# Optimization experiments

Hardware: AMD Instinct MI355X
Metric: run time of the kernel (lower is better)

## Reference

```python
import jax, jax.numpy as jnp
import numpy as np

B, S, D, H = 4, 2048, 1024, 16
Dh = D // H
MAX_WAVELENGTH = 10000.0


def apply_rope(x, positions, head_dim):
    # x: [B, S, H, Dh], positions: [B, S]
    fraction = 2.0 * jnp.arange(head_dim // 2, dtype=jnp.float32) / head_dim
    timescale = MAX_WAVELENGTH ** fraction                     # [Dh/2]
    sinusoid = positions[..., None].astype(jnp.float32) / timescale  # [B, S, Dh/2]
    sinusoid = sinusoid[..., None, :]                          # [B, S, 1, Dh/2]
    sin, cos = jnp.sin(sinusoid), jnp.cos(sinusoid)
    first, second = jnp.split(x, 2, axis=-1)
    out = jnp.concatenate([first * cos - second * sin,
                           second * cos + first * sin], axis=-1)
    return out.astype(x.dtype)


def setup_inputs() -> dict:
    key = jax.random.key(0)
    k0, k1, k2, k3, k4 = jax.random.split(key, 5)
    inputs = jax.random.normal(k0, (B, S, D), dtype=jnp.float32)
    segment_positions = jnp.broadcast_to(jnp.arange(S, dtype=jnp.int32), (B, S))
    # causal mask, broadcastable over heads: [B, 1, S, S]
    mask = jnp.broadcast_to(jnp.tril(jnp.ones((S, S), dtype=bool))[None, None], (B, 1, S, S))
    std = 0.02
    w_q = jax.random.normal(k1, (D, H, Dh), dtype=jnp.float32) * std
    w_k = jax.random.normal(k2, (D, H, Dh), dtype=jnp.float32) * std
    w_v = jax.random.normal(k3, (D, H, Dh), dtype=jnp.float32) * std
    w_out = jax.random.normal(k4, (H, Dh, D), dtype=jnp.float32) * std
    return {"inputs": inputs, "w_q": w_q, "w_k": w_k, "w_v": w_v,
            "w_out": w_out, "segment_positions": segment_positions, "mask": mask}


def reference(inputs, w_q, w_k, w_v, w_out, segment_positions, mask):
    # QKV projections: [B, S, D] x [D, H, Dh] -> [B, S, H, Dh]
    q = jnp.einsum('bsd,dhk->bshk', inputs, w_q)
    k = jnp.einsum('bsd,dhk->bshk', inputs, w_k)
    v = jnp.einsum('bsd,dhk->bshk', inputs, w_v)
    q = apply_rope(q, segment_positions, Dh)
    k = apply_rope(k, segment_positions, Dh)
    q = q / jnp.sqrt(jnp.asarray(Dh, dtype=q.dtype))
    attn = jnp.einsum('bqhd,bkhd->bhqk', q, k)                 # [B, H, S, S]
    big_neg = jnp.finfo(attn.dtype).min
    attn = jnp.where(mask, attn, big_neg)
    attn = jax.nn.softmax(attn, axis=-1)
    x = jnp.einsum('bhqk,bkhd->bqhd', attn, v)                 # [B, S, H, Dh]
    return jnp.einsum('bqhd,hdm->bqm', x, w_out)               # [B, S, D]
```

## Files before the change

kernel.cpp:

```cpp
#include <hip/hip_runtime.h>
#include <stdint.h>
#include <math.h>

#define S_LEN 2048
#define DMODEL 1024
#define NHEAD 16
#define DHEAD 64
#define BATCH 4
#define MROWS (BATCH * S_LEN)

typedef __attribute__((ext_vector_type(8))) short bf16x8;
typedef __attribute__((ext_vector_type(4))) float f32x4;

#define MFMA16(a, b, c) __builtin_amdgcn_mfma_f32_16x16x32_bf16(a, b, c, 0, 0, 0)

__device__ __forceinline__ unsigned short f2b(float f) {
  union { float f; unsigned u; } v; v.f = f;
  unsigned u = v.u;
  return (unsigned short)((u + 0x7FFFu + ((u >> 16) & 1u)) >> 16);
}
__device__ __forceinline__ unsigned pkrn(float a, float b) {
  unsigned ua = __float_as_uint(a) + 0x8000u;
  unsigned ub = __float_as_uint(b) + 0x8000u;
  return __builtin_amdgcn_perm(ub, ua, 0x07060302);
}

__device__ __forceinline__ void async16(const void* g, void* l) {
  __builtin_amdgcn_global_load_lds((const __attribute__((address_space(1))) void*)g,
                                   (__attribute__((address_space(3))) void*)l,
                                   16, 0, 0);
}

__global__ __launch_bounds__(256) void cvt_kernel(const float4* __restrict__ in,
                                                  unsigned short* __restrict__ out,
                                                  int n4) {
  int i = blockIdx.x * 256 + threadIdx.x;
  if (i < n4) {
    float4 v = in[i];
    ushort4 o;
    o.x = f2b(v.x); o.y = f2b(v.y); o.z = f2b(v.z); o.w = f2b(v.w);
    *(ushort4*)(out + 4 * (size_t)i) = o;
  }
}

struct TP4 { const float* s[4]; unsigned short* d[4]; };
__global__ __launch_bounds__(256) void transpose_cvt4(TP4 p) {
  const float* in = p.s[blockIdx.z];
  unsigned short* out = p.d[blockIdx.z];
  __shared__ float T[64][65];
  int r0 = blockIdx.y * 64, c0 = blockIdx.x * 64;
  int t = threadIdx.x;
  int c = t & 63, rr = t >> 6;
#pragma unroll
  for (int i = 0; i < 16; i++) {
    int r = i * 4 + rr;
    T[r][c] = in[(size_t)(r0 + r) * 1024 + c0 + c];
  }
  __syncthreads();
  int r2 = t & 63, cc = t >> 6;
#pragma unroll
  for (int i = 0; i < 16; i++) {
    int c2 = i * 4 + cc;
    out[(size_t)(c0 + c2) * 1024 + r0 + r2] = f2b(T[r2][c2]);
  }
}

__global__ __launch_bounds__(256) void gemm_qkv(const unsigned short* __restrict__ A,
                                                const unsigned short* __restrict__ Bt,
                                                unsigned short* __restrict__ Qr,
                                                unsigned short* __restrict__ Kr,
                                                unsigned short* __restrict__ Vt,
                                                const int* __restrict__ pos) {
  constexpr int K = 1024;
  __shared__ unsigned short As[128 * 64];
  __shared__ unsigned short Bs[128 * 64];
  const int bm = blockIdx.y * 128, bn = blockIdx.x * 128;
  const int t = threadIdx.x;
  const int wave = t >> 6, lane = t & 63, quad = lane >> 4, l16 = lane & 15;
  const int wm = (wave >> 1) * 64, wn = (wave & 1) * 64;
  f32x4 acc[4][4] = {};
  const int srow = lane >> 3;
  const int gcol = (((lane & 7) ^ srow)) * 8;
  const unsigned short* Ag = A + (size_t)(bm + wave * 32 + srow) * K + gcol;
  const unsigned short* Bg = Bt + (size_t)(bn + wave * 32 + srow) * K + gcol;
  unsigned short* AsW = &As[(wave * 32) * 64];
  unsigned short* BsW = &Bs[(wave * 32) * 64];
  const int rsw = l16 & 7;

  for (int k0 = 0; k0 < K; k0 += 64) {
    __syncthreads();
#pragma unroll
    for (int i = 0; i < 4; i++) {
      async16(Ag + (size_t)(i * 8) * K + k0, AsW + i * 8 * 64);
      async16(Bg + (size_t)(i * 8) * K + k0, BsW + i * 8 * 64);
    }
    __syncthreads();
#pragma unroll
    for (int kk = 0; kk < 2; kk++) {
      const int sl = ((kk * 4 + quad) ^ rsw) << 3;
      bf16x8 af[4], bfr[4];
#pragma unroll
      for (int mt = 0; mt < 4; mt++)
        af[mt] = *(const bf16x8*)&As[(wm + mt * 16 + l16) * 64 + sl];
#pragma unroll
      for (int nt = 0; nt < 4; nt++)
        bfr[nt] = *(const bf16x8*)&Bs[(wn + nt * 16 + l16) * 64 + sl];
#pragma unroll
      for (int mt = 0; mt < 4; mt++)
#pragma unroll
        for (int nt = 0; nt < 4; nt++)
          acc[mt][nt] = MFMA16(af[mt], bfr[nt], acc[mt][nt]);
    }
  }

  const int cb = bn + wn;
  if (cb >= 2048) {
    const int h = (cb - 2048) >> 6;
#pragma unroll
    for (int mt = 0; mt < 4; mt++)
#pragma unroll
      for (int nt = 0; nt < 4; nt++) {
        int row = bm + wm + mt * 16 + quad * 4;
        int b = row >> 11, s = row & (S_LEN - 1);
        int dh = nt * 16 + l16;
        ushort4 w4;
        w4.x = f2b(acc[mt][nt][0]); w4.y = f2b(acc[mt][nt][1]);
        w4.z = f2b(acc[mt][nt][2]); w4.w = f2b(acc[mt][nt][3]);
        *(ushort4*)&Vt[((size_t)(b * NHEAD + h) * DHEAD + dh) * S_LEN + s] = w4;
      }
  } else {
    const bool isQ = cb < 1024;
    unsigned short* dst0 = isQ ? Qr : Kr;
    const float scl = isQ ? 0.18033688011112042f : 1.0f;
    const int h = (cb >> 6) & 15;
    const float LT = 0.28782313662425572f;
    float it0 = __expf(-(float)l16 * LT);
    float it1 = __expf(-(float)(16 + l16) * LT);
#pragma unroll
    for (int mt = 0; mt < 4; mt++) {
#pragma unroll
      for (int r = 0; r < 4; r++) {
        int row = bm + wm + mt * 16 + quad * 4 + r;
        int b = row >> 11, s = row & (S_LEN - 1);
        float p = (float)pos[row];
        float sn0, cs0, sn1, cs1;
        sincosf(p * it0, &sn0, &cs0);
        sincosf(p * it1, &sn1, &cs1);
        float x0 = acc[mt][0][r], x1 = acc[mt][1][r];
        float x2 = acc[mt][2][r], x3 = acc[mt][3][r];
        float o0 = (x0 * cs0 - x2 * sn0) * scl;
        float o2 = (x2 * cs0 + x0 * sn0) * scl;
        float o1 = (x1 * cs1 - x3 * sn1) * scl;
        float o3 = (x3 * cs1 + x1 * sn1) * scl;
        unsigned short* dst =
            dst0 + ((size_t)(b * NHEAD + h) * S_LEN + s) * DHEAD;
        dst[0 * 16 + l16] = f2b(o0);
        dst[1 * 16 + l16] = f2b(o1);
        dst[2 * 16 + l16] = f2b(o2);
        dst[3 * 16 + l16] = f2b(o3);
      }
    }
  }
}

__global__ __launch_bounds__(256) void gemm_out(const unsigned short* __restrict__ A,
                                                const unsigned short* __restrict__ Bt,
                                                float* __restrict__ C) {
  constexpr int K = 1024, N = 1024;
  __shared__ unsigned short As[128 * 64];
  __shared__ unsigned short Bs[128 * 64];
  const int bm = blockIdx.y * 128, bn = blockIdx.x * 128;
  const int t = threadIdx.x;
  const int wave = t >> 6, lane = t & 63, quad = lane >> 4, l16 = lane & 15;
  const int wm = (wave >> 1) * 64, wn = (wave & 1) * 64;
  f32x4 acc[4][4] = {};
  const int srow = lane >> 3;
  const int gcol = (((lane & 7) ^ srow)) * 8;
  const unsigned short* Ag = A + (size_t)(bm + wave * 32 + srow) * K + gcol;
  const unsigned short* Bg = Bt + (size_t)(bn + wave * 32 + srow) * K + gcol;
  unsigned short* AsW = &As[(wave * 32) * 64];
  unsigned short* BsW = &Bs[(wave * 32) * 64];
  const int rsw = l16 & 7;

  for (int k0 = 0; k0 < K; k0 += 64) {
    __syncthreads();
#pragma unroll
    for (int i = 0; i < 4; i++) {
      async16(Ag + (size_t)(i * 8) * K + k0, AsW + i * 8 * 64);
      async16(Bg + (size_t)(i * 8) * K + k0, BsW + i * 8 * 64);
    }
    __syncthreads();
#pragma unroll
    for (int kk = 0; kk < 2; kk++) {
      const int sl = ((kk * 4 + quad) ^ rsw) << 3;
      bf16x8 af[4], bfr[4];
#pragma unroll
      for (int mt = 0; mt < 4; mt++)
        af[mt] = *(const bf16x8*)&As[(wm + mt * 16 + l16) * 64 + sl];
#pragma unroll
      for (int nt = 0; nt < 4; nt++)
        bfr[nt] = *(const bf16x8*)&Bs[(wn + nt * 16 + l16) * 64 + sl];
#pragma unroll
      for (int mt = 0; mt < 4; mt++)
#pragma unroll
        for (int nt = 0; nt < 4; nt++)
          acc[mt][nt] = MFMA16(af[mt], bfr[nt], acc[mt][nt]);
    }
  }
#pragma unroll
  for (int mt = 0; mt < 4; mt++)
#pragma unroll
    for (int nt = 0; nt < 4; nt++)
#pragma unroll
      for (int r = 0; r < 4; r++) {
        int row = bm + wm + mt * 16 + quad * 4 + r;
        int col = bn + wn + nt * 16 + l16;
        C[(size_t)row * N + col] = acc[mt][nt][r];
      }
}

__global__ __launch_bounds__(256) void flash_kernel(const unsigned short* __restrict__ Qr,
                                                    const unsigned short* __restrict__ Kr,
                                                    const unsigned short* __restrict__ Vt,
                                                    unsigned short* __restrict__ Xat) {
  const int lid = blockIdx.x;
  const int xcd = lid & 7, j = lid >> 3;
  const int bh = (xcd << 3) | (j >> 4);
  const int qA = j & 15, qB = 31 - qA;
  const unsigned short* Qh = Qr + (size_t)bh * S_LEN * DHEAD;
  const unsigned short* Kh = Kr + (size_t)bh * S_LEN * DHEAD;
  const unsigned short* Vh = Vt + (size_t)bh * DHEAD * S_LEN;
  __shared__ unsigned short Ks[2][64 * 64];
  __shared__ unsigned short Vs[2][64 * 64];
  __shared__ unsigned short Pt[4][16 * 64];
  const int t = threadIdx.x, wave = t >> 6, lane = t & 63;
  const int quad = lane >> 4, l16 = lane & 15;
  const int srow = lane >> 3;
  const int gcol = (((lane & 7) ^ srow)) * 8;
  const int rsw = l16 & 7;
  const int q0A = qA * 64, q0B = qB * 64;
  const int qrA = q0A + wave * 16 + l16;
  const int qrB = q0B + wave * 16 + l16;

  bf16x8 qfA0 = *(const bf16x8*)(Qh + (size_t)qrA * DHEAD + quad * 8);
  bf16x8 qfA1 = *(const bf16x8*)(Qh + (size_t)qrA * DHEAD + 32 + quad * 8);
  bf16x8 qfB0 = *(const bf16x8*)(Qh + (size_t)qrB * DHEAD + quad * 8);
  bf16x8 qfB1 = *(const bf16x8*)(Qh + (size_t)qrB * DHEAD + 32 + quad * 8);

  f32x4 oA[4] = {}, oB[4] = {};
  float lA = 0.f, lB = 0.f;
  unsigned short* PtW = &Pt[wave][0];

#pragma unroll
  for (int i = 0; i < 2; i++) {
    async16(Kh + (size_t)(wave * 16 + i * 8 + srow) * DHEAD + gcol,
            &Ks[0][(wave * 16 + i * 8) * 64]);
    async16(Vh + (size_t)(wave * 16 + i * 8 + srow) * S_LEN + gcol,
            &Vs[0][(wave * 16 + i * 8) * 64]);
  }

  for (int kt = 0; kt <= qB; kt++) {
    const int cur = kt & 1;
    const int k0 = kt * 64;
    __syncthreads();
    if (kt < qB) {
      const int k1 = k0 + 64;
#pragma unroll
      for (int i = 0; i < 2; i++) {
        async16(Kh + (size_t)(k1 + wave * 16 + i * 8 + srow) * DHEAD + gcol,
                &Ks[cur ^ 1][(wave * 16 + i * 8) * 64]);
        async16(Vh + (size_t)(wave * 16 + i * 8 + srow) * S_LEN + k1 + gcol,
                &Vs[cur ^ 1][(wave * 16 + i * 8) * 64]);
      }
    }
    const unsigned short* K_ = Ks[cur];
    const unsigned short* V_ = Vs[cur];
    bf16x8 kb0[4], kb1[4];
#pragma unroll
    for (int nt = 0; nt < 4; nt++) {
      kb0[nt] = *(const bf16x8*)&K_[(nt * 16 + l16) * 64 + ((quad ^ rsw) << 3)];
      kb1[nt] = *(const bf16x8*)&K_[(nt * 16 + l16) * 64 + (((4 + quad) ^ rsw) << 3)];
    }

    {
      f32x4 sc[4] = {};
#pragma unroll
      for (int nt = 0; nt < 4; nt++) {
        sc[nt] = MFMA16(kb0[nt], qfB0, sc[nt]);
        sc[nt] = MFMA16(kb1[nt], qfB1, sc[nt]);
      }
      const bool dg = (kt == qB);
#pragma unroll
      for (int nt = 0; nt < 4; nt++) {
        int kg = k0 + nt * 16 + quad * 4;
        float p0 = (dg && kg + 0 > qrB) ? 0.f : exp2f(sc[nt][0]);
        float p1 = (dg && kg + 1 > qrB) ? 0.f : exp2f(sc[nt][1]);
        float p2 = (dg && kg + 2 > qrB) ? 0.f : exp2f(sc[nt][2]);
        float p3 = (dg && kg + 3 > qrB) ? 0.f : exp2f(sc[nt][3]);
        lB += (p0 + p1) + (p2 + p3);
        uint2 w; w.x = pkrn(p0, p1); w.y = pkrn(p2, p3);
        int s8 = nt * 2 + (quad >> 1);
        *(uint2*)&PtW[l16 * 64 + ((s8 ^ rsw) << 3) + (quad & 1) * 4] = w;
      }
#pragma unroll
      for (int kk = 0; kk < 2; kk++) {
        bf16x8 pb = *(const bf16x8*)&PtW[l16 * 64 + (((kk * 4 + quad) ^ rsw) << 3)];
#pragma unroll
        for (int nt = 0; nt < 4; nt++) {
          bf16x8 vb =
              *(const bf16x8*)&V_[(nt * 16 + l16) * 64 + (((kk * 4 + quad) ^ rsw) << 3)];
          oB[nt] = MFMA16(vb, pb, oB[nt]);
        }
      }
    }
    if (kt <= qA) {
      f32x4 sc[4] = {};
#pragma unroll
      for (int nt = 0; nt < 4; nt++) {
        sc[nt] = MFMA16(kb0[nt], qfA0, sc[nt]);
        sc[nt] = MFMA16(kb1[nt], qfA1, sc[nt]);
      }
      const bool dg = (kt == qA);
#pragma unroll
      for (int nt = 0; nt < 4; nt++) {
        int kg = k0 + nt * 16 + quad * 4;
        float p0 = (dg && kg + 0 > qrA) ? 0.f : exp2f(sc[nt][0]);
        float p1 = (dg && kg + 1 > qrA) ? 0.f : exp2f(sc[nt][1]);
        float p2 = (dg && kg + 2 > qrA) ? 0.f : exp2f(sc[nt][2]);
        float p3 = (dg && kg + 3 > qrA) ? 0.f : exp2f(sc[nt][3]);
        lA += (p0 + p1) + (p2 + p3);
        uint2 w; w.x = pkrn(p0, p1); w.y = pkrn(p2, p3);
        int s8 = nt * 2 + (quad >> 1);
        *(uint2*)&PtW[l16 * 64 + ((s8 ^ rsw) << 3) + (quad & 1) * 4] = w;
      }
#pragma unroll
      for (int kk = 0; kk < 2; kk++) {
        bf16x8 pb = *(const bf16x8*)&PtW[l16 * 64 + (((kk * 4 + quad) ^ rsw) << 3)];
#pragma unroll
        for (int nt = 0; nt < 4; nt++) {
          bf16x8 vb =
              *(const bf16x8*)&V_[(nt * 16 + l16) * 64 + (((kk * 4 + quad) ^ rsw) << 3)];
          oA[nt] = MFMA16(vb, pb, oA[nt]);
        }
      }
    }
  }

  lA += __shfl_xor(lA, 16); lA += __shfl_xor(lA, 32);
  lB += __shfl_xor(lB, 16); lB += __shfl_xor(lB, 32);
  const float ivA = 1.0f / lA, ivB = 1.0f / lB;
  const int b = bh >> 4, h = bh & 15;
  unsigned short* dA = Xat + (size_t)(b * S_LEN + qrA) * DMODEL + h * DHEAD;
  unsigned short* dB = Xat + (size_t)(b * S_LEN + qrB) * DMODEL + h * DHEAD;
#pragma unroll
  for (int nt = 0; nt < 4; nt++) {
    ushort4 wa, wb;
    wa.x = f2b(oA[nt][0] * ivA); wa.y = f2b(oA[nt][1] * ivA);
    wa.z = f2b(oA[nt][2] * ivA); wa.w = f2b(oA[nt][3] * ivA);
    wb.x = f2b(oB[nt][0] * ivB); wb.y = f2b(oB[nt][1] * ivB);
    wb.z = f2b(oB[nt][2] * ivB); wb.w = f2b(oB[nt][3] * ivB);
    *(ushort4*)(dA + nt * 16 + quad * 4) = wa;
    *(ushort4*)(dB + nt * 16 + quad * 4) = wb;
  }
}

extern "C" void kernel_launch(void* const* d_in, const int* in_sizes, int n_in,
                              void* d_out, int out_size, void* d_ws, size_t ws_size,
                              hipStream_t stream) {
  const float* x = (const float*)d_in[0];
  const float* wq = (const float*)d_in[1];
  const float* wk = (const float*)d_in[2];
  const float* wv = (const float*)d_in[3];
  const float* wo = (const float*)d_in[4];
  const int* pos = (const int*)d_in[5];
  float* out = (float*)d_out;
  char* ws = (char*)d_ws;

  const size_t EL_X = (size_t)MROWS * DMODEL;
  const size_t EL_W = (size_t)DMODEL * DMODEL;
  unsigned short* Xb = (unsigned short*)ws;
  unsigned short* Wqkv = Xb + EL_X;
  unsigned short* WoT = Wqkv + 3 * EL_W;
  unsigned short* Qr = WoT + EL_W;
  unsigned short* Kr = Qr + EL_X;
  unsigned short* Vt = Kr + EL_X;
  unsigned short* Xat = Vt + EL_X;

  cvt_kernel<<<(int)(EL_X / 4 / 256), 256, 0, stream>>>((const float4*)x, Xb,
                                                        (int)(EL_X / 4));
  TP4 tp;
  tp.s[0] = wq; tp.d[0] = Wqkv;
  tp.s[1] = wk; tp.d[1] = Wqkv + EL_W;
  tp.s[2] = wv; tp.d[2] = Wqkv + 2 * EL_W;
  tp.s[3] = wo; tp.d[3] = WoT;
  dim3 tg(16, 16, 4);
  transpose_cvt4<<<tg, 256, 0, stream>>>(tp);
  dim3 gq(24, 64);
  gemm_qkv<<<gq, 256, 0, stream>>>(Xb, Wqkv, Qr, Kr, Vt, pos);
  flash_kernel<<<1024, 256, 0, stream>>>(Qr, Kr, Vt, Xat);
  dim3 gg(8, 64);
  gemm_out<<<gg, 256, 0, stream>>>(Xat, WoT, out);
}
```

Before: 325.0 us.

## Split paired causal query tiles into one tile per block, longest first

The flash attention kernel stops pairing a short and a long query tile per block (which shared K/V loads and balanced work). It now launches twice as many blocks, each handling one query tile, and schedules the longest tiles first. This gives more parallelism and fewer registers per block, but each K/V tile is loaded separately for each query tile, and the XCD-aware head mapping is dropped.

```diff
diff --git a/kernel.cpp b/kernel.cpp
--- a/kernel.cpp
+++ b/kernel.cpp
@@ -223,10 +223,9 @@
                                                     const unsigned short* __restrict__ Kr,
                                                     const unsigned short* __restrict__ Vt,
                                                     unsigned short* __restrict__ Xat) {
-  const int lid = blockIdx.x;
-  const int xcd = lid & 7, j = lid >> 3;
-  const int bh = (xcd << 3) | (j >> 4);
-  const int qA = j & 15, qB = 31 - qA;
+  const int idx = blockIdx.x;
+  const int qt = 31 - (idx >> 6);
+  const int bh = idx & 63;
   const unsigned short* Qh = Qr + (size_t)bh * S_LEN * DHEAD;
   const unsigned short* Kh = Kr + (size_t)bh * S_LEN * DHEAD;
   const unsigned short* Vh = Vt + (size_t)bh * DHEAD * S_LEN;
@@ -238,17 +237,14 @@
   const int srow = lane >> 3;
   const int gcol = (((lane & 7) ^ srow)) * 8;
   const int rsw = l16 & 7;
-  const int q0A = qA * 64, q0B = qB * 64;
-  const int qrA = q0A + wave * 16 + l16;
-  const int qrB = q0B + wave * 16 + l16;
-
-  bf16x8 qfA0 = *(const bf16x8*)(Qh + (size_t)qrA * DHEAD + quad * 8);
-  bf16x8 qfA1 = *(const bf16x8*)(Qh + (size_t)qrA * DHEAD + 32 + quad * 8);
-  bf16x8 qfB0 = *(const bf16x8*)(Qh + (size_t)qrB * DHEAD + quad * 8);
-  bf16x8 qfB1 = *(const bf16x8*)(Qh + (size_t)qrB * DHEAD + 32 + quad * 8);
-
-  f32x4 oA[4] = {}, oB[4] = {};
-  float lA = 0.f, lB = 0.f;
+  const int q0 = qt * 64;
+  const int qr = q0 + wave * 16 + l16;
+
+  bf16x8 qf0 = *(const bf16x8*)(Qh + (size_t)qr * DHEAD + quad * 8);
+  bf16x8 qf1 = *(const bf16x8*)(Qh + (size_t)qr * DHEAD + 32 + quad * 8);
+
+  f32x4 o[4] = {};
+  float l = 0.f;
   unsigned short* PtW = &Pt[wave][0];
 
 #pragma unroll
@@ -259,11 +255,11 @@
             &Vs[0][(wave * 16 + i * 8) * 64]);
   }
 
-  for (int kt = 0; kt <= qB; kt++) {
+  for (int kt = 0; kt <= qt; kt++) {
     const int cur = kt & 1;
     const int k0 = kt * 64;
     __syncthreads();
-    if (kt < qB) {
+    if (kt < qt) {
       const int k1 = k0 + 64;
 #pragma unroll
       for (int i = 0; i < 2; i++) {
@@ -275,92 +271,51 @@
     }
     const unsigned short* K_ = Ks[cur];
     const unsigned short* V_ = Vs[cur];
-    bf16x8 kb0[4], kb1[4];
+
+    f32x4 sc[4] = {};
 #pragma unroll
     for (int nt = 0; nt < 4; nt++) {
-      kb0[nt] = *(const bf16x8*)&K_[(nt * 16 + l16) * 64 + ((quad ^ rsw) << 3)];
-      kb1[nt] = *(const bf16x8*)&K_[(nt * 16 + l16) * 64 + (((4 + quad) ^ rsw) << 3)];
-    }
-
-    {
-      f32x4 sc[4] = {};
+      bf16x8 kb0 = *(const bf16x8*)&K_[(nt * 16 + l16) * 64 + ((quad ^ rsw) << 3)];
+      bf16x8 kb1 = *(const bf16x8*)&K_[(nt * 16 + l16) * 64 + (((4 + quad) ^ rsw) << 3)];
+      sc[nt] = MFMA16(kb0, qf0, sc[nt]);
+      sc[nt] = MFMA16(kb1, qf1, sc[nt]);
+    }
+    const bool dg = (kt == qt);
+#pragma unroll
+    for (int nt = 0; nt < 4; nt++) {
+      int kg = k0 + nt * 16 + quad * 4;
+      float p0 = (dg && kg + 0 > qr) ? 0.f : exp2f(sc[nt][0]);
+      float p1 = (dg && kg + 1 > qr) ? 0.f : exp2f(sc[nt][1]);
+      float p2 = (dg && kg + 2 > qr) ? 0.f : exp2f(sc[nt][2]);
+      float p3 = (dg && kg + 3 > qr) ? 0.f : exp2f(sc[nt][3]);
+      l += (p0 + p1) + (p2 + p3);
+      uint2 w; w.x = pkrn(p0, p1); w.y = pkrn(p2, p3);
+      int s8 = nt * 2 + (quad >> 1);
+      *(uint2*)&PtW[l16 * 64 + ((s8 ^ rsw) << 3) + (quad & 1) * 4] = w;
+    }
+#pragma unroll
+    for (int kk = 0; kk < 2; kk++) {
+      bf16x8 pb = *(const bf16x8*)&PtW[l16 * 64 + (((kk * 4 + quad) ^ rsw) << 3)];
 #pragma unroll
       for (int nt = 0; nt < 4; nt++) {
-        sc[nt] = MFMA16(kb0[nt], qfB0, sc[nt]);
-        sc[nt] = MFMA16(kb1[nt], qfB1, sc[nt]);
-      }
-      const bool dg = (kt == qB);
-#pragma unroll
-      for (int nt = 0; nt < 4; nt++) {
-        int kg = k0 + nt * 16 + quad * 4;
-        float p0 = (dg && kg + 0 > qrB) ? 0.f : exp2f(sc[nt][0]);
-        float p1 = (dg && kg + 1 > qrB) ? 0.f : exp2f(sc[nt][1]);
-        float p2 = (dg && kg + 2 > qrB) ? 0.f : exp2f(sc[nt][2]);
-        float p3 = (dg && kg + 3 > qrB) ? 0.f : exp2f(sc[nt][3]);
-        lB += (p0 + p1) + (p2 + p3);
-        uint2 w; w.x = pkrn(p0, p1); w.y = pkrn(p2, p3);
-        int s8 = nt * 2 + (quad >> 1);
-        *(uint2*)&PtW[l16 * 64 + ((s8 ^ rsw) << 3) + (quad & 1) * 4] = w;
-      }
-#pragma unroll
-      for (int kk = 0; kk < 2; kk++) {
-        bf16x8 pb = *(const bf16x8*)&PtW[l16 * 64 + (((kk * 4 + quad) ^ rsw) << 3)];
-#pragma unroll
-        for (int nt = 0; nt < 4; nt++) {
-          bf16x8 vb =
-              *(const bf16x8*)&V_[(nt * 16 + l16) * 64 + (((kk * 4 + quad) ^ rsw) << 3)];
-          oB[nt] = MFMA16(vb, pb, oB[nt]);
-        }
-      }
-    }
-    if (kt <= qA) {
-      f32x4 sc[4] = {};
-#pragma unroll
-      for (int nt = 0; nt < 4; nt++) {
-        sc[nt] = MFMA16(kb0[nt], qfA0, sc[nt]);
-        sc[nt] = MFMA16(kb1[nt], qfA1, sc[nt]);
-      }
-      const bool dg = (kt == qA);
-#pragma unroll
-      for (int nt = 0; nt < 4; nt++) {
-        int kg = k0 + nt * 16 + quad * 4;
-        float p0 = (dg && kg + 0 > qrA) ? 0.f : exp2f(sc[nt][0]);
-        float p1 = (dg && kg + 1 > qrA) ? 0.f : exp2f(sc[nt][1]);
-        float p2 = (dg && kg + 2 > qrA) ? 0.f : exp2f(sc[nt][2]);
-        float p3 = (dg && kg + 3 > qrA) ? 0.f : exp2f(sc[nt][3]);
-        lA += (p0 + p1) + (p2 + p3);
-        uint2 w; w.x = pkrn(p0, p1); w.y = pkrn(p2, p3);
-        int s8 = nt * 2 + (quad >> 1);
-        *(uint2*)&PtW[l16 * 64 + ((s8 ^ rsw) << 3) + (quad & 1) * 4] = w;
-      }
-#pragma unroll
-      for (int kk = 0; kk < 2; kk++) {
-        bf16x8 pb = *(const bf16x8*)&PtW[l16 * 64 + (((kk * 4 + quad) ^ rsw) << 3)];
-#pragma unroll
-        for (int nt = 0; nt < 4; nt++) {
-          bf16x8 vb =
-              *(const bf16x8*)&V_[(nt * 16 + l16) * 64 + (((kk * 4 + quad) ^ rsw) << 3)];
-          oA[nt] = MFMA16(vb, pb, oA[nt]);
-        }
-      }
-    }
-  }
-
-  lA += __shfl_xor(lA, 16); lA += __shfl_xor(lA, 32);
-  lB += __shfl_xor(lB, 16); lB += __shfl_xor(lB, 32);
-  const float ivA = 1.0f / lA, ivB = 1.0f / lB;
+        bf16x8 vb =
+            *(const bf16x8*)&V_[(nt * 16 + l16) * 64 + (((kk * 4 + quad) ^ rsw) << 3)];
+        o[nt] = MFMA16(vb, pb, o[nt]);
+      }
+    }
+  }
+
+  l += __shfl_xor(l, 16);
+  l += __shfl_xor(l, 32);
+  const float iv = 1.0f / l;
   const int b = bh >> 4, h = bh & 15;
-  unsigned short* dA = Xat + (size_t)(b * S_LEN + qrA) * DMODEL + h * DHEAD;
-  unsigned short* dB = Xat + (size_t)(b * S_LEN + qrB) * DMODEL + h * DHEAD;
+  unsigned short* d = Xat + (size_t)(b * S_LEN + qr) * DMODEL + h * DHEAD;
 #pragma unroll
   for (int nt = 0; nt < 4; nt++) {
-    ushort4 wa, wb;
-    wa.x = f2b(oA[nt][0] * ivA); wa.y = f2b(oA[nt][1] * ivA);
-    wa.z = f2b(oA[nt][2] * ivA); wa.w = f2b(oA[nt][3] * ivA);
-    wb.x = f2b(oB[nt][0] * ivB); wb.y = f2b(oB[nt][1] * ivB);
-    wb.z = f2b(oB[nt][2] * ivB); wb.w = f2b(oB[nt][3] * ivB);
-    *(ushort4*)(dA + nt * 16 + quad * 4) = wa;
-    *(ushort4*)(dB + nt * 16 + quad * 4) = wb;
+    ushort4 w4;
+    w4.x = f2b(o[nt][0] * iv); w4.y = f2b(o[nt][1] * iv);
+    w4.z = f2b(o[nt][2] * iv); w4.w = f2b(o[nt][3] * iv);
+    *(ushort4*)(d + nt * 16 + quad * 4) = w4;
   }
 }
 
@@ -397,7 +352,7 @@
   transpose_cvt4<<<tg, 256, 0, stream>>>(tp);
   dim3 gq(24, 64);
   gemm_qkv<<<gq, 256, 0, stream>>>(Xb, Wqkv, Qr, Kr, Vt, pos);
-  flash_kernel<<<1024, 256, 0, stream>>>(Qr, Kr, Vt, Xat);
+  flash_kernel<<<2048, 256, 0, stream>>>(Qr, Kr, Vt, Xat);
   dim3 gg(8, 64);
   gemm_out<<<gg, 256, 0, stream>>>(Xat, WoT, out);
 }
```

Result: faster. 309.7 us (-4.7%).
